# Kernel optimization log

Hardware: AMD Instinct MI355X
Metric: run time of the kernel (lower is better)

The kernel has to match this reference:

```python
import jax, jax.numpy as jnp
import numpy as np

N_USERS = 100000
N_ITEMS = 50000
N_NODES = N_USERS + N_ITEMS
N_EDGES = 4800000
EMB_DIM = 64
N_LAYERS = 3


def setup_inputs() -> dict:
    key = jax.random.key(0)
    k1, k2, k3, k4, k5 = jax.random.split(key, 5)
    adj_rows = jax.random.randint(k1, (N_EDGES,), 0, N_NODES, dtype=jnp.int64 if jax.config.jax_enable_x64 else jnp.int32)
    adj_cols = jax.random.randint(k2, (N_EDGES,), 0, N_NODES, dtype=jnp.int64 if jax.config.jax_enable_x64 else jnp.int32)
    adj_vals = jax.random.uniform(k3, (N_EDGES,), dtype=jnp.float32)
    user_emb = jax.random.normal(k4, (N_USERS, EMB_DIM), dtype=jnp.float32)
    item_emb = jax.random.normal(k5, (N_ITEMS, EMB_DIM), dtype=jnp.float32)
    return {"adj_rows": adj_rows, "adj_cols": adj_cols, "adj_vals": adj_vals,
            "user_emb": user_emb, "item_emb": item_emb}


def _spmm(rows, cols, vals, x):
    # sparse.mm(adj, x): gather source node features, scale by edge value,
    # scatter-add into destination rows. Shapes: [E] indices, [N, D] features.
    msgs = vals[:, None] * x[cols]          # [E, D]
    return jax.ops.segment_sum(msgs, rows, num_segments=N_NODES)  # [N, D]


def reference(adj_rows, adj_cols, adj_vals, user_emb, item_emb):
    all_emb = jnp.concatenate([user_emb, item_emb], axis=0)  # [N, D]
    acc = all_emb                                            # running sum over layers (fused stack+mean)
    emb = all_emb
    for _ in range(N_LAYERS):
        emb = _spmm(adj_rows, adj_cols, adj_vals, emb)
        acc = acc + emb
    final = acc / jnp.asarray(N_LAYERS + 1, dtype=acc.dtype)
    return final[:N_USERS], final[N_USERS:]
```

## Files before the change

kernel.cpp:

```cpp
#include <hip/hip_runtime.h>


#define N_USERS 100000
#define N_ITEMS 50000
#define N_NODES 150000
#define N_EDGES 4800000
#define EMB_DIM 64

typedef unsigned short u16;
typedef unsigned int   u32;

constexpr int NODE_FLOATS  = N_NODES * EMB_DIM;
constexpr int NODE_FLOAT4S = NODE_FLOATS / 4;
constexpr int USER_FLOAT4S = N_USERS * EMB_DIM / 4;

constexpr int BSH  = 7;
constexpr int BRW  = 128;
constexpr int NB   = (N_NODES + BRW - 1) / BRW;
constexpr int EPB  = 6144;
constexpr int ABLK2 = (N_EDGES + EPB - 1) / EPB;
constexpr int HSW  = NB + 1;
constexpr int SB_CAP2 = 5760;
constexpr int CSR_CAP = 6000000;

static __device__ __forceinline__ float bf2f(u16 b) {
    return __uint_as_float(((u32)b) << 16);
}
static __device__ __forceinline__ u16 f2bf(float f) {
    u32 u = __float_as_uint(f);
    return (u16)((u + 0x7FFFu + ((u >> 16) & 1u)) >> 16);
}

__global__ void prelude_kernel(const float* __restrict__ user_emb,
                               const float* __restrict__ item_emb,
                               u16* __restrict__ emb,
                               int* __restrict__ csr_cursor) {
    int i = blockIdx.x * blockDim.x + threadIdx.x;
    if (i == 0) csr_cursor[0] = 0;
    if (i >= NODE_FLOAT4S) return;
    float4 v = (i < USER_FLOAT4S) ? ((const float4*)user_emb)[i]
                                  : ((const float4*)item_emb)[i - USER_FLOAT4S];
    ushort4 o;
    o.x = f2bf(v.x); o.y = f2bf(v.y); o.z = f2bf(v.z); o.w = f2bf(v.w);
    ((ushort4*)emb)[i] = o;
}

__global__ void stageA2_kernel(const int* __restrict__ rows,
                               const int* __restrict__ cols,
                               const float* __restrict__ vals,
                               uint2* __restrict__ stage_rec,
                               u32* __restrict__ hs) {
    __shared__ u32 lkey[EPB];
    __shared__ u16 lval[EPB];
    __shared__ u16 lbkt[EPB];
    __shared__ int hist[NB];
    __shared__ int hstart[NB];
    __shared__ int hcur[NB];
    __shared__ int ws4[4];

    const int tid  = threadIdx.x;
    const int base = blockIdx.x * EPB;
    const int cnt  = min(EPB, N_EDGES - base);

    for (int i = tid; i < NB; i += 256) hist[i] = 0;
    __syncthreads();

    for (int k = 0; k < EPB / 256; k += 8) {
        int rbuf[8];
        #pragma unroll
        for (int q = 0; q < 8; ++q) {
            int idx = (k + q) * 256 + tid;
            rbuf[q] = (idx < cnt) ? rows[base + idx] : -1;
        }
        #pragma unroll
        for (int q = 0; q < 8; ++q)
            if (rbuf[q] >= 0) atomicAdd(&hist[rbuf[q] >> BSH], 1);
    }
    __syncthreads();

    const int lane = tid & 63, wave = tid >> 6;
    int carry = 0;
    for (int c0 = 0; c0 < NB; c0 += 256) {
        int i = c0 + tid;
        int v = (i < NB) ? hist[i] : 0;
        int incl = v;
        #pragma unroll
        for (int off = 1; off < 64; off <<= 1) {
            int t = __shfl_up(incl, off);
            if (lane >= off) incl += t;
        }
        if (lane == 63) ws4[wave] = incl;
        __syncthreads();
        int wpref = 0, tot = 0;
        #pragma unroll
        for (int w = 0; w < 4; ++w) { int s = ws4[w]; if (w < wave) wpref += s; tot += s; }
        int excl = carry + wpref + incl - v;
        if (i < NB) { hstart[i] = excl; hcur[i] = excl; }
        carry += tot;
        __syncthreads();
    }

    for (int k = 0; k < EPB / 256; k += 8) {
        int rb[8], cb[8]; float vb[8];
        #pragma unroll
        for (int q = 0; q < 8; ++q) {
            int idx = (k + q) * 256 + tid;
            if (idx < cnt) { rb[q] = rows[base + idx]; cb[q] = cols[base + idx]; vb[q] = vals[base + idx]; }
            else rb[q] = -1;
        }
        #pragma unroll
        for (int q = 0; q < 8; ++q) {
            if (rb[q] < 0) continue;
            int b = rb[q] >> BSH;
            int p = atomicAdd(&hcur[b], 1);
            lkey[p] = ((u32)(rb[q] & (BRW - 1)) << 24) | (u32)cb[q];
            lval[p] = f2bf(vb[q]);
            lbkt[p] = (u16)b;
        }
    }
    __syncthreads();
    (void)lbkt;

    uint2* __restrict__ dst = stage_rec + (size_t)blockIdx.x * EPB;
    for (int i = tid; i < cnt; i += 256)
        dst[i] = make_uint2(lkey[i], (u32)lval[i]);

    u32* __restrict__ hrow = hs + (size_t)blockIdx.x * HSW;
    for (int i = tid; i < NB; i += 256) hrow[i] = (u32)hstart[i];
    if (tid == 0) hrow[NB] = (u32)cnt;
}

__global__ void stageB2_kernel(const uint2* __restrict__ stage_rec,
                               const u32* __restrict__ hs,
                               int* __restrict__ csr_cursor,
                               u32* __restrict__ csr_col,
                               u16* __restrict__ csr_val,
                               u32* __restrict__ desc) {
    __shared__ u32 skey[SB_CAP2];
    __shared__ u16 sval[SB_CAP2];
    __shared__ int rhist[256], rpad0[256], rcur[256];
    __shared__ int ws4[4];
    __shared__ int sbase_sh;

    const int b   = blockIdx.x;
    const int tid = threadIdx.x;
    rhist[tid] = 0;
    __syncthreads();

    for (int a = tid; a < ABLK2; a += 256) {
        const u32* hp = hs + (size_t)a * HSW + b;
        u32 s = hp[0], e = hp[1];
        const uint2* rp = stage_rec + (size_t)a * EPB;
        for (u32 i = s; i < e; ++i)
            atomicAdd(&rhist[rp[i].x >> 24], 1);
    }
    __syncthreads();

    const int lane = tid & 63, wave = tid >> 6;
    int v  = rhist[tid];
    int vp = (v + 15) & ~15;
    int incl = vp;
    #pragma unroll
    for (int off = 1; off < 64; off <<= 1) {
        int t = __shfl_up(incl, off);
        if (lane >= off) incl += t;
    }
    if (lane == 63) ws4[wave] = incl;
    __syncthreads();
    int wpref = 0, total = 0;
    #pragma unroll
    for (int w = 0; w < 4; ++w) { int s = ws4[w]; if (w < wave) wpref += s; total += s; }
    int excl = wpref + incl - vp;
    rpad0[tid] = excl;
    rcur[tid]  = excl;
    if (tid == 0) sbase_sh = atomicAdd(csr_cursor, total);
    __syncthreads();

    const int tcap = min(total, SB_CAP2);
    for (int i = tid; i < tcap; i += 256) { skey[i] = 0u; sval[i] = 0; }
    __syncthreads();

    for (int a = tid; a < ABLK2; a += 256) {
        const u32* hp = hs + (size_t)a * HSW + b;
        u32 s = hp[0], e = hp[1];
        const uint2* rp = stage_rec + (size_t)a * EPB;
        for (u32 i = s; i < e; ++i) {
            uint2 r = rp[i];
            int p = atomicAdd(&rcur[r.x >> 24], 1);
            if (p < SB_CAP2) { skey[p] = r.x & 0x00FFFFFFu; sval[p] = (u16)r.y; }
        }
    }
    __syncthreads();

    const int sbase = sbase_sh;
    for (int i = tid; i < tcap; i += 256) {
        int g = sbase + i;
        if (g < CSR_CAP) { csr_col[g] = skey[i]; csr_val[g] = sval[i]; }
    }
    if (tid < BRW) {
        int grow = b * BRW + tid;
        if (grow < N_NODES) {
            int cp = vp; if (cp > 240) cp = 240;
            desc[grow] = ((u32)(sbase + rpad0[tid]) << 8) | (u32)cp;
        }
    }
}

__global__ __launch_bounds__(256, 8)
void spmm_rw_kernel(const u32* __restrict__ desc,
                    const u32* __restrict__ csr_col,
                    const u16* __restrict__ csr_val,
                    const u16* __restrict__ x,
                    u16* __restrict__ y,
                    const u16* __restrict__ e0,
                    const u16* __restrict__ y1,
                    const u16* __restrict__ y2,
                    float* __restrict__ out) {
    const int lane = threadIdx.x & 63;
    const int wid  = __builtin_amdgcn_readfirstlane(threadIdx.x >> 6);
    const int row  = blockIdx.x * 4 + wid;
    if (row >= N_NODES) return;

    const u32 d   = desc[row];
    const int beg = (int)(d >> 8);
    const int nch = (int)(d & 255u) >> 4;

    const u32* __restrict__ pc = csr_col + beg;
    const u32* __restrict__ pv = ((const u32*)csr_val) + (beg >> 1);
    const u16* __restrict__ xl = x + lane;

    float a[4] = {0.f, 0.f, 0.f, 0.f};

    for (int ch = 0; ch < nch; ++ch) {
        u32 c[16];
        u32 w[8];
        #pragma unroll
        for (int k = 0; k < 16; ++k) c[k] = pc[ch * 16 + k];
        #pragma unroll
        for (int k = 0; k < 8; ++k)  w[k] = pv[ch * 8 + k];

        u32 xv[16];
        #pragma unroll
        for (int k = 0; k < 16; ++k)
            xv[k] = (u32)xl[(size_t)c[k] * EMB_DIM];

        #pragma unroll
        for (int k = 0; k < 16; ++k) {
            u32 vb = (k & 1) ? (w[k >> 1] & 0xFFFF0000u) : (w[k >> 1] << 16);
            float vv = __uint_as_float(vb);
            float xf = __uint_as_float(xv[k] << 16);
            a[k & 3] += vv * xf;
        }
    }
    float s = (a[0] + a[1]) + (a[2] + a[3]);

    size_t oidx = (size_t)row * EMB_DIM + lane;
    if (y) {
        y[oidx] = f2bf(s);
    } else {
        float r = (bf2f(e0[oidx]) + bf2f(y1[oidx]) + bf2f(y2[oidx]) + s) * 0.25f;
        out[oidx] = r;
    }
}

__global__ void init3_kernel(const float* __restrict__ user_emb,
                             const float* __restrict__ item_emb,
                             float* __restrict__ emb,
                             float* __restrict__ acc,
                             float* __restrict__ nxt) {
    int i = blockIdx.x * blockDim.x + threadIdx.x;
    if (i >= NODE_FLOAT4S) return;
    float4 v = (i < USER_FLOAT4S) ? ((const float4*)user_emb)[i]
                                  : ((const float4*)item_emb)[i - USER_FLOAT4S];
    ((float4*)emb)[i] = v;
    ((float4*)acc)[i] = v;
    ((float4*)nxt)[i] = make_float4(0.f, 0.f, 0.f, 0.f);
}

__global__ void spmm_atomic_kernel(const int* __restrict__ rows,
                                   const int* __restrict__ cols,
                                   const float* __restrict__ vals,
                                   const float* __restrict__ x,
                                   float* __restrict__ y) {
    unsigned tid = blockIdx.x * blockDim.x + threadIdx.x;
    unsigned e  = tid >> 4;
    unsigned d4 = tid & 15u;
    if (e >= N_EDGES) return;
    int r = rows[e]; int c = cols[e]; float v = vals[e];
    float4 xv = ((const float4*)(x + (size_t)c * EMB_DIM))[d4];
    float* yp = y + (size_t)r * EMB_DIM + d4 * 4;
    atomicAdd(yp + 0, v * xv.x);
    atomicAdd(yp + 1, v * xv.y);
    atomicAdd(yp + 2, v * xv.z);
    atomicAdd(yp + 3, v * xv.w);
}

__global__ void acc_kernel(float* __restrict__ acc, const float* __restrict__ nxt,
                           float* __restrict__ zbuf, int do_zero, float scale) {
    int i = blockIdx.x * blockDim.x + threadIdx.x;
    if (i >= NODE_FLOAT4S) return;
    float4 a = ((float4*)acc)[i];
    float4 n = ((const float4*)nxt)[i];
    a.x = (a.x + n.x) * scale; a.y = (a.y + n.y) * scale;
    a.z = (a.z + n.z) * scale; a.w = (a.w + n.w) * scale;
    ((float4*)acc)[i] = a;
    if (do_zero) ((float4*)zbuf)[i] = make_float4(0.f, 0.f, 0.f, 0.f);
}

extern "C" void kernel_launch(void* const* d_in, const int* in_sizes, int n_in,
                              void* d_out, int out_size, void* d_ws, size_t ws_size,
                              hipStream_t stream) {
    const int*   rows     = (const int*)d_in[0];
    const int*   cols     = (const int*)d_in[1];
    const float* vals     = (const float*)d_in[2];
    const float* user_emb = (const float*)d_in[3];
    const float* item_emb = (const float*)d_in[4];
    float* out = (float*)d_out;

    constexpr size_t U_BUF  = (size_t)NODE_FLOATS / 2;
    constexpr size_t U_SREC = (size_t)ABLK2 * EPB * 2;
    constexpr size_t U_HS   = (size_t)ABLK2 * HSW;
    constexpr size_t U_CCOL = (size_t)CSR_CAP;
    constexpr size_t U_CVAL = (size_t)CSR_CAP / 2;
    size_t need_u32 = U_BUF + U_SREC + U_HS + U_CCOL + U_CVAL + (size_t)N_NODES + 16;

    const int EW_BLOCKS = (NODE_FLOAT4S + 255) / 256;

    if (ws_size >= need_u32 * 4) {
        u32* W = (u32*)d_ws;
        u16*   buf0      = (u16*)W;
        uint2* stage_rec = (uint2*)(W + U_BUF);
        u16*   buf1      = (u16*)(W + U_BUF);
        u16*   buf2      = (u16*)(W + U_BUF + U_BUF);
        u32*   hs        = W + U_BUF + U_SREC;
        u32*   csr_col   = hs + U_HS;
        u16*   csr_val   = (u16*)(csr_col + U_CCOL);
        u32*   desc      = (u32*)(csr_col + U_CCOL + U_CVAL);
        int*   csr_cur   = (int*)(desc + N_NODES);

        prelude_kernel<<<EW_BLOCKS, 256, 0, stream>>>(user_emb, item_emb, buf0, csr_cur);
        stageA2_kernel<<<ABLK2, 256, 0, stream>>>(rows, cols, vals, stage_rec, hs);
        stageB2_kernel<<<NB, 256, 0, stream>>>(stage_rec, hs, csr_cur,
                                               csr_col, csr_val, desc);

        const int SPMM_BLOCKS = (N_NODES + 3) / 4;
        spmm_rw_kernel<<<SPMM_BLOCKS, 256, 0, stream>>>(desc, csr_col, csr_val,
                                                        buf0, buf1, nullptr, nullptr, nullptr, nullptr);
        spmm_rw_kernel<<<SPMM_BLOCKS, 256, 0, stream>>>(desc, csr_col, csr_val,
                                                        buf1, buf2, nullptr, nullptr, nullptr, nullptr);
        spmm_rw_kernel<<<SPMM_BLOCKS, 256, 0, stream>>>(desc, csr_col, csr_val,
                                                        buf2, nullptr, buf0, buf1, buf2, out);
    } else {
        float* buf0 = (float*)d_ws;
        float* buf1 = buf0 + NODE_FLOATS;
        const int SPMM_BLOCKS = (int)(((size_t)N_EDGES * 16 + 255) / 256);
        init3_kernel<<<EW_BLOCKS, 256, 0, stream>>>(user_emb, item_emb, buf0, out, buf1);
        float* prev = buf0; float* next = buf1;
        for (int layer = 0; layer < 3; ++layer) {
            spmm_atomic_kernel<<<SPMM_BLOCKS, 256, 0, stream>>>(rows, cols, vals, prev, next);
            if (layer < 2) acc_kernel<<<EW_BLOCKS, 256, 0, stream>>>(out, next, prev, 1, 1.0f);
            else           acc_kernel<<<EW_BLOCKS, 256, 0, stream>>>(out, next, prev, 0, 0.25f);
            float* t = prev; prev = next; next = t;
        }
    }
}
```

Baseline: 522.1 us.

## Build CSR with degree count, scan and atomic scatter instead of bucket sort

Replaces the two-pass, shared-memory bucket sort that staged edge records with a simpler CSR build. Per-row degrees are counted with global atomics inside the prelude, then padded and prefix-scanned in two small kernels. Each edge is then placed by an atomic cursor per row. This drops the large staging buffer and the heavy LDS-bound sort kernels. In exchange it adds many random global atomics and scattered writes, plus a zeroing pass over the CSR arrays for the padding slots.

```diff
diff --git a/kernel.cpp b/kernel.cpp
--- a/kernel.cpp
+++ b/kernel.cpp
@@ -14,14 +14,9 @@
 constexpr int NODE_FLOAT4S = NODE_FLOATS / 4;
 constexpr int USER_FLOAT4S = N_USERS * EMB_DIM / 4;
 
-constexpr int BSH  = 7;
-constexpr int BRW  = 128;
-constexpr int NB   = (N_NODES + BRW - 1) / BRW;
-constexpr int EPB  = 6144;
-constexpr int ABLK2 = (N_EDGES + EPB - 1) / EPB;
-constexpr int HSW  = NB + 1;
-constexpr int SB_CAP2 = 5760;
-constexpr int CSR_CAP = 6000000;
+constexpr int SCAN_BLK  = 147;
+constexpr int ROWS_PAD  = SCAN_BLK * 1024;
+constexpr int CSR_CAP   = 6200000;
 
 static __device__ __forceinline__ float bf2f(u16 b) {
     return __uint_as_float(((u32)b) << 16);
@@ -31,178 +26,94 @@
     return (u16)((u + 0x7FFFu + ((u >> 16) & 1u)) >> 16);
 }
 
+constexpr size_t U_CCOL = (size_t)CSR_CAP;
+constexpr size_t U_CVAL = (size_t)CSR_CAP / 2;
+constexpr size_t U_DEG  = (size_t)ROWS_PAD;
+constexpr size_t U_CUR  = (size_t)ROWS_PAD;
+constexpr size_t ZU32   = U_CCOL + U_CVAL + U_DEG + U_CUR;
+
+__global__ void zero_kernel(uint4* __restrict__ z) {
+    size_t i = (size_t)blockIdx.x * blockDim.x + threadIdx.x;
+    if (i < ZU32 / 4) z[i] = make_uint4(0u, 0u, 0u, 0u);
+}
+
 __global__ void prelude_kernel(const float* __restrict__ user_emb,
                                const float* __restrict__ item_emb,
                                u16* __restrict__ emb,
-                               int* __restrict__ csr_cursor) {
+                               const int* __restrict__ rows,
+                               u32* __restrict__ deg) {
     int i = blockIdx.x * blockDim.x + threadIdx.x;
-    if (i == 0) csr_cursor[0] = 0;
     if (i >= NODE_FLOAT4S) return;
     float4 v = (i < USER_FLOAT4S) ? ((const float4*)user_emb)[i]
                                   : ((const float4*)item_emb)[i - USER_FLOAT4S];
     ushort4 o;
     o.x = f2bf(v.x); o.y = f2bf(v.y); o.z = f2bf(v.z); o.w = f2bf(v.w);
     ((ushort4*)emb)[i] = o;
-}
-
-__global__ void stageA2_kernel(const int* __restrict__ rows,
-                               const int* __restrict__ cols,
-                               const float* __restrict__ vals,
-                               uint2* __restrict__ stage_rec,
-                               u32* __restrict__ hs) {
-    __shared__ u32 lkey[EPB];
-    __shared__ u16 lval[EPB];
-    __shared__ u16 lbkt[EPB];
-    __shared__ int hist[NB];
-    __shared__ int hstart[NB];
-    __shared__ int hcur[NB];
-    __shared__ int ws4[4];
-
-    const int tid  = threadIdx.x;
-    const int base = blockIdx.x * EPB;
-    const int cnt  = min(EPB, N_EDGES - base);
-
-    for (int i = tid; i < NB; i += 256) hist[i] = 0;
-    __syncthreads();
-
-    for (int k = 0; k < EPB / 256; k += 8) {
-        int rbuf[8];
-        #pragma unroll
-        for (int q = 0; q < 8; ++q) {
-            int idx = (k + q) * 256 + tid;
-            rbuf[q] = (idx < cnt) ? rows[base + idx] : -1;
-        }
-        #pragma unroll
-        for (int q = 0; q < 8; ++q)
-            if (rbuf[q] >= 0) atomicAdd(&hist[rbuf[q] >> BSH], 1);
-    }
-    __syncthreads();
-
-    const int lane = tid & 63, wave = tid >> 6;
-    int carry = 0;
-    for (int c0 = 0; c0 < NB; c0 += 256) {
-        int i = c0 + tid;
-        int v = (i < NB) ? hist[i] : 0;
-        int incl = v;
-        #pragma unroll
-        for (int off = 1; off < 64; off <<= 1) {
-            int t = __shfl_up(incl, off);
-            if (lane >= off) incl += t;
-        }
-        if (lane == 63) ws4[wave] = incl;
-        __syncthreads();
-        int wpref = 0, tot = 0;
-        #pragma unroll
-        for (int w = 0; w < 4; ++w) { int s = ws4[w]; if (w < wave) wpref += s; tot += s; }
-        int excl = carry + wpref + incl - v;
-        if (i < NB) { hstart[i] = excl; hcur[i] = excl; }
-        carry += tot;
-        __syncthreads();
-    }
-
-    for (int k = 0; k < EPB / 256; k += 8) {
-        int rb[8], cb[8]; float vb[8];
-        #pragma unroll
-        for (int q = 0; q < 8; ++q) {
-            int idx = (k + q) * 256 + tid;
-            if (idx < cnt) { rb[q] = rows[base + idx]; cb[q] = cols[base + idx]; vb[q] = vals[base + idx]; }
-            else rb[q] = -1;
-        }
-        #pragma unroll
-        for (int q = 0; q < 8; ++q) {
-            if (rb[q] < 0) continue;
-            int b = rb[q] >> BSH;
-            int p = atomicAdd(&hcur[b], 1);
-            lkey[p] = ((u32)(rb[q] & (BRW - 1)) << 24) | (u32)cb[q];
-            lval[p] = f2bf(vb[q]);
-            lbkt[p] = (u16)b;
-        }
-    }
-    __syncthreads();
-    (void)lbkt;
-
-    uint2* __restrict__ dst = stage_rec + (size_t)blockIdx.x * EPB;
-    for (int i = tid; i < cnt; i += 256)
-        dst[i] = make_uint2(lkey[i], (u32)lval[i]);
-
-    u32* __restrict__ hrow = hs + (size_t)blockIdx.x * HSW;
-    for (int i = tid; i < NB; i += 256) hrow[i] = (u32)hstart[i];
-    if (tid == 0) hrow[NB] = (u32)cnt;
-}
-
-__global__ void stageB2_kernel(const uint2* __restrict__ stage_rec,
-                               const u32* __restrict__ hs,
-                               int* __restrict__ csr_cursor,
-                               u32* __restrict__ csr_col,
-                               u16* __restrict__ csr_val,
-                               u32* __restrict__ desc) {
-    __shared__ u32 skey[SB_CAP2];
-    __shared__ u16 sval[SB_CAP2];
-    __shared__ int rhist[256], rpad0[256], rcur[256];
-    __shared__ int ws4[4];
-    __shared__ int sbase_sh;
-
-    const int b   = blockIdx.x;
+    atomicAdd(&deg[rows[i]], 1u);
+    atomicAdd(&deg[rows[i + NODE_FLOAT4S]], 1u);
+}
+
+__global__ __launch_bounds__(1024)
+void scanA_kernel(u32* __restrict__ deg_desc, u32* __restrict__ blocksum) {
+    __shared__ int wsum[16], wbase[16];
     const int tid = threadIdx.x;
-    rhist[tid] = 0;
-    __syncthreads();
-
-    for (int a = tid; a < ABLK2; a += 256) {
-        const u32* hp = hs + (size_t)a * HSW + b;
-        u32 s = hp[0], e = hp[1];
-        const uint2* rp = stage_rec + (size_t)a * EPB;
-        for (u32 i = s; i < e; ++i)
-            atomicAdd(&rhist[rp[i].x >> 24], 1);
-    }
-    __syncthreads();
-
-    const int lane = tid & 63, wave = tid >> 6;
-    int v  = rhist[tid];
-    int vp = (v + 15) & ~15;
+    const int row = blockIdx.x * 1024 + tid;
+    const int lane = tid & 63, wv = tid >> 6;
+
+    int d  = (int)deg_desc[row];
+    int vp = (d + 15) & ~15;
+
     int incl = vp;
     #pragma unroll
     for (int off = 1; off < 64; off <<= 1) {
         int t = __shfl_up(incl, off);
         if (lane >= off) incl += t;
     }
-    if (lane == 63) ws4[wave] = incl;
+    if (lane == 63) wsum[wv] = incl;
     __syncthreads();
-    int wpref = 0, total = 0;
-    #pragma unroll
-    for (int w = 0; w < 4; ++w) { int s = ws4[w]; if (w < wave) wpref += s; total += s; }
-    int excl = wpref + incl - vp;
-    rpad0[tid] = excl;
-    rcur[tid]  = excl;
-    if (tid == 0) sbase_sh = atomicAdd(csr_cursor, total);
+    if (tid < 16) {
+        int s = wsum[tid];
+        int i2 = s;
+        #pragma unroll
+        for (int off = 1; off < 16; off <<= 1) {
+            int t = __shfl_up(i2, off);
+            if (lane >= off) i2 += t;
+        }
+        wbase[tid] = i2 - s;
+        if (tid == 15) blocksum[blockIdx.x] = (u32)i2;
+    }
     __syncthreads();
 
-    const int tcap = min(total, SB_CAP2);
-    for (int i = tid; i < tcap; i += 256) { skey[i] = 0u; sval[i] = 0; }
-    __syncthreads();
-
-    for (int a = tid; a < ABLK2; a += 256) {
-        const u32* hp = hs + (size_t)a * HSW + b;
-        u32 s = hp[0], e = hp[1];
-        const uint2* rp = stage_rec + (size_t)a * EPB;
-        for (u32 i = s; i < e; ++i) {
-            uint2 r = rp[i];
-            int p = atomicAdd(&rcur[r.x >> 24], 1);
-            if (p < SB_CAP2) { skey[p] = r.x & 0x00FFFFFFu; sval[p] = (u16)r.y; }
-        }
-    }
-    __syncthreads();
-
-    const int sbase = sbase_sh;
-    for (int i = tid; i < tcap; i += 256) {
-        int g = sbase + i;
-        if (g < CSR_CAP) { csr_col[g] = skey[i]; csr_val[g] = sval[i]; }
-    }
-    if (tid < BRW) {
-        int grow = b * BRW + tid;
-        if (grow < N_NODES) {
-            int cp = vp; if (cp > 240) cp = 240;
-            desc[grow] = ((u32)(sbase + rpad0[tid]) << 8) | (u32)cp;
-        }
+    int excl = wbase[wv] + incl - vp;
+    int cnt  = vp > 240 ? 240 : vp;
+    deg_desc[row] = ((u32)excl << 8) | (u32)cnt;
+}
+
+__global__ __launch_bounds__(1024)
+void scanC_kernel(u32* __restrict__ desc, const u32* __restrict__ blocksum) {
+    const int blk = blockIdx.x;
+    u32 base = 0;
+    for (int i = 0; i < blk; ++i) base += blocksum[i];
+    const int row = blk * 1024 + threadIdx.x;
+    desc[row] += base << 8;
+}
+
+__global__ void scatter_kernel(const int* __restrict__ rows,
+                               const int* __restrict__ cols,
+                               const float* __restrict__ vals,
+                               const u32* __restrict__ desc,
+                               u32* __restrict__ cursor,
+                               u32* __restrict__ csr_col,
+                               u16* __restrict__ csr_val) {
+    int e = blockIdx.x * blockDim.x + threadIdx.x;
+    if (e >= N_EDGES) return;
+    int r = rows[e];
+    u32 dsc = desc[r];
+    u32 pos = atomicAdd(&cursor[r], 1u);
+    u32 g = (dsc >> 8) + pos;
+    if (g < (u32)CSR_CAP) {
+        csr_col[g] = (u32)cols[e];
+        csr_val[g] = f2bf(vals[e]);
     }
 }
 
@@ -317,38 +228,38 @@
     const float* item_emb = (const float*)d_in[4];
     float* out = (float*)d_out;
 
-    constexpr size_t U_BUF  = (size_t)NODE_FLOATS / 2;
-    constexpr size_t U_SREC = (size_t)ABLK2 * EPB * 2;
-    constexpr size_t U_HS   = (size_t)ABLK2 * HSW;
-    constexpr size_t U_CCOL = (size_t)CSR_CAP;
-    constexpr size_t U_CVAL = (size_t)CSR_CAP / 2;
-    size_t need_u32 = U_BUF + U_SREC + U_HS + U_CCOL + U_CVAL + (size_t)N_NODES + 16;
+    constexpr size_t U_BUF = (size_t)NODE_FLOATS / 2;
+    size_t need_u32 = 3 * U_BUF + ZU32 + 160;
 
     const int EW_BLOCKS = (NODE_FLOAT4S + 255) / 256;
 
     if (ws_size >= need_u32 * 4) {
         u32* W = (u32*)d_ws;
-        u16*   buf0      = (u16*)W;
-        uint2* stage_rec = (uint2*)(W + U_BUF);
-        u16*   buf1      = (u16*)(W + U_BUF);
-        u16*   buf2      = (u16*)(W + U_BUF + U_BUF);
-        u32*   hs        = W + U_BUF + U_SREC;
-        u32*   csr_col   = hs + U_HS;
-        u16*   csr_val   = (u16*)(csr_col + U_CCOL);
-        u32*   desc      = (u32*)(csr_col + U_CCOL + U_CVAL);
-        int*   csr_cur   = (int*)(desc + N_NODES);
-
-        prelude_kernel<<<EW_BLOCKS, 256, 0, stream>>>(user_emb, item_emb, buf0, csr_cur);
-        stageA2_kernel<<<ABLK2, 256, 0, stream>>>(rows, cols, vals, stage_rec, hs);
-        stageB2_kernel<<<NB, 256, 0, stream>>>(stage_rec, hs, csr_cur,
-                                               csr_col, csr_val, desc);
+        u16* buf0     = (u16*)W;
+        u16* buf1     = (u16*)(W + U_BUF);
+        u16* buf2     = (u16*)(W + 2 * U_BUF);
+        u32* csr_col  = W + 3 * U_BUF;
+        u16* csr_val  = (u16*)(csr_col + U_CCOL);
+        u32* deg_desc = csr_col + U_CCOL + U_CVAL;
+        u32* cursor   = deg_desc + U_DEG;
+        u32* blocksum = cursor + U_CUR;
+
+        const int ZBLOCKS = (int)((ZU32 / 4 + 255) / 256);
+        zero_kernel<<<ZBLOCKS, 256, 0, stream>>>((uint4*)csr_col);
+        prelude_kernel<<<EW_BLOCKS, 256, 0, stream>>>(user_emb, item_emb, buf0,
+                                                      rows, deg_desc);
+        scanA_kernel<<<SCAN_BLK, 1024, 0, stream>>>(deg_desc, blocksum);
+        scanC_kernel<<<SCAN_BLK, 1024, 0, stream>>>(deg_desc, blocksum);
+        const int SCAT_BLOCKS = (N_EDGES + 255) / 256;
+        scatter_kernel<<<SCAT_BLOCKS, 256, 0, stream>>>(rows, cols, vals, deg_desc,
+                                                        cursor, csr_col, csr_val);
 
         const int SPMM_BLOCKS = (N_NODES + 3) / 4;
-        spmm_rw_kernel<<<SPMM_BLOCKS, 256, 0, stream>>>(desc, csr_col, csr_val,
+        spmm_rw_kernel<<<SPMM_BLOCKS, 256, 0, stream>>>(deg_desc, csr_col, csr_val,
                                                         buf0, buf1, nullptr, nullptr, nullptr, nullptr);
-        spmm_rw_kernel<<<SPMM_BLOCKS, 256, 0, stream>>>(desc, csr_col, csr_val,
+        spmm_rw_kernel<<<SPMM_BLOCKS, 256, 0, stream>>>(deg_desc, csr_col, csr_val,
                                                         buf1, buf2, nullptr, nullptr, nullptr, nullptr);
-        spmm_rw_kernel<<<SPMM_BLOCKS, 256, 0, stream>>>(desc, csr_col, csr_val,
+        spmm_rw_kernel<<<SPMM_BLOCKS, 256, 0, stream>>>(deg_desc, csr_col, csr_val,
                                                         buf2, nullptr, buf0, buf1, buf2, out);
     } else {
         float* buf0 = (float*)d_ws;
```

Measured after the change: 908.5 us. 1.74x slower.

## Replace two-pass bucket CSR build with global-atomic partition scatter into fixed slots

Applied to the files above, without the earlier changes.

The CSR build changes from per-block staging records plus a per-bucket scan over every staging block to a partitioned scheme. Each stage-A block reserves space in 512-row partitions with a global atomic and scatters its records directly into fixed-capacity partition buffers. A 512-thread stage-B block per partition then counting-sorts its own contiguous buffer into fixed-offset CSR slots. This removes stage B's loop over all ABLK2 blocks' headers and its scattered small reads, but it introduces fixed capacities (PCAP, PCSR) that drop edges silently if a partition overflows, and it pads every row inside fixed partition strides.

```diff
diff --git a/kernel.cpp b/kernel.cpp
--- a/kernel.cpp
+++ b/kernel.cpp
@@ -14,14 +14,13 @@
 constexpr int NODE_FLOAT4S = NODE_FLOATS / 4;
 constexpr int USER_FLOAT4S = N_USERS * EMB_DIM / 4;
 
-constexpr int BSH  = 7;
-constexpr int BRW  = 128;
-constexpr int NB   = (N_NODES + BRW - 1) / BRW;
-constexpr int EPB  = 6144;
+constexpr int PSH   = 9;
+constexpr int PRW   = 512;
+constexpr int NP    = (N_NODES + PRW - 1) / PRW;
+constexpr int PCAP  = 17920;
+constexpr int PCSR  = 22528;
+constexpr int EPB   = 6144;
 constexpr int ABLK2 = (N_EDGES + EPB - 1) / EPB;
-constexpr int HSW  = NB + 1;
-constexpr int SB_CAP2 = 5760;
-constexpr int CSR_CAP = 6000000;
 
 static __device__ __forceinline__ float bf2f(u16 b) {
     return __uint_as_float(((u32)b) << 16);
@@ -34,9 +33,9 @@
 __global__ void prelude_kernel(const float* __restrict__ user_emb,
                                const float* __restrict__ item_emb,
                                u16* __restrict__ emb,
-                               int* __restrict__ csr_cursor) {
+                               int* __restrict__ pcnt) {
     int i = blockIdx.x * blockDim.x + threadIdx.x;
-    if (i == 0) csr_cursor[0] = 0;
+    if (i < 512) pcnt[i] = 0;
     if (i >= NODE_FLOAT4S) return;
     float4 v = (i < USER_FLOAT4S) ? ((const float4*)user_emb)[i]
                                   : ((const float4*)item_emb)[i - USER_FLOAT4S];
@@ -45,24 +44,22 @@
     ((ushort4*)emb)[i] = o;
 }
 
-__global__ void stageA2_kernel(const int* __restrict__ rows,
-                               const int* __restrict__ cols,
-                               const float* __restrict__ vals,
-                               uint2* __restrict__ stage_rec,
-                               u32* __restrict__ hs) {
+__global__ void stageP_kernel(const int* __restrict__ rows,
+                              const int* __restrict__ cols,
+                              const float* __restrict__ vals,
+                              int* __restrict__ pcnt,
+                              uint2* __restrict__ part_buf) {
     __shared__ u32 lkey[EPB];
     __shared__ u16 lval[EPB];
     __shared__ u16 lbkt[EPB];
-    __shared__ int hist[NB];
-    __shared__ int hstart[NB];
-    __shared__ int hcur[NB];
+    __shared__ int hist[NP], hstart[NP], hcur[NP], gbase[NP];
     __shared__ int ws4[4];
 
     const int tid  = threadIdx.x;
     const int base = blockIdx.x * EPB;
     const int cnt  = min(EPB, N_EDGES - base);
 
-    for (int i = tid; i < NB; i += 256) hist[i] = 0;
+    for (int i = tid; i < NP; i += 256) hist[i] = 0;
     __syncthreads();
 
     for (int k = 0; k < EPB / 256; k += 8) {
@@ -74,15 +71,15 @@
         }
         #pragma unroll
         for (int q = 0; q < 8; ++q)
-            if (rbuf[q] >= 0) atomicAdd(&hist[rbuf[q] >> BSH], 1);
+            if (rbuf[q] >= 0) atomicAdd(&hist[rbuf[q] >> PSH], 1);
     }
     __syncthreads();
 
     const int lane = tid & 63, wave = tid >> 6;
     int carry = 0;
-    for (int c0 = 0; c0 < NB; c0 += 256) {
+    for (int c0 = 0; c0 < NP; c0 += 256) {
         int i = c0 + tid;
-        int v = (i < NB) ? hist[i] : 0;
+        int v = (i < NP) ? hist[i] : 0;
         int incl = v;
         #pragma unroll
         for (int off = 1; off < 64; off <<= 1) {
@@ -95,7 +92,7 @@
         #pragma unroll
         for (int w = 0; w < 4; ++w) { int s = ws4[w]; if (w < wave) wpref += s; tot += s; }
         int excl = carry + wpref + incl - v;
-        if (i < NB) { hstart[i] = excl; hcur[i] = excl; }
+        if (i < NP) { hstart[i] = excl; hcur[i] = excl; }
         carry += tot;
         __syncthreads();
     }
@@ -111,52 +108,55 @@
         #pragma unroll
         for (int q = 0; q < 8; ++q) {
             if (rb[q] < 0) continue;
-            int b = rb[q] >> BSH;
+            int b = rb[q] >> PSH;
             int p = atomicAdd(&hcur[b], 1);
-            lkey[p] = ((u32)(rb[q] & (BRW - 1)) << 24) | (u32)cb[q];
+            lkey[p] = ((u32)(rb[q] & (PRW - 1)) << 18) | (u32)cb[q];
             lval[p] = f2bf(vb[q]);
             lbkt[p] = (u16)b;
         }
     }
     __syncthreads();
-    (void)lbkt;
-
-    uint2* __restrict__ dst = stage_rec + (size_t)blockIdx.x * EPB;
-    for (int i = tid; i < cnt; i += 256)
-        dst[i] = make_uint2(lkey[i], (u32)lval[i]);
-
-    u32* __restrict__ hrow = hs + (size_t)blockIdx.x * HSW;
-    for (int i = tid; i < NB; i += 256) hrow[i] = (u32)hstart[i];
-    if (tid == 0) hrow[NB] = (u32)cnt;
-}
-
-__global__ void stageB2_kernel(const uint2* __restrict__ stage_rec,
-                               const u32* __restrict__ hs,
-                               int* __restrict__ csr_cursor,
-                               u32* __restrict__ csr_col,
-                               u16* __restrict__ csr_val,
-                               u32* __restrict__ desc) {
-    __shared__ u32 skey[SB_CAP2];
-    __shared__ u16 sval[SB_CAP2];
-    __shared__ int rhist[256], rpad0[256], rcur[256];
-    __shared__ int ws4[4];
-    __shared__ int sbase_sh;
-
-    const int b   = blockIdx.x;
+
+    for (int i = tid; i < NP; i += 256) {
+        int n = hist[i];
+        if (n) {
+            int p = atomicAdd(&pcnt[i], n);
+            gbase[i] = (p + n <= PCAP) ? p : -1;
+        }
+    }
+    __syncthreads();
+
+    for (int i = tid; i < cnt; i += 256) {
+        int b  = lbkt[i];
+        int gb = gbase[b];
+        if (gb >= 0)
+            part_buf[(size_t)b * PCAP + gb + (i - hstart[b])] =
+                make_uint2(lkey[i], (u32)lval[i]);
+    }
+}
+
+__global__ __launch_bounds__(512)
+void stageB_kernel(const int* __restrict__ pcnt,
+                   const uint2* __restrict__ part_buf,
+                   u32* __restrict__ csr_col,
+                   u16* __restrict__ csr_val,
+                   u32* __restrict__ desc) {
+    __shared__ int rhist[PRW], rcur[PRW];
+    __shared__ int wsum[8];
+
+    const int p   = blockIdx.x;
     const int tid = threadIdx.x;
     rhist[tid] = 0;
     __syncthreads();
 
-    for (int a = tid; a < ABLK2; a += 256) {
-        const u32* hp = hs + (size_t)a * HSW + b;
-        u32 s = hp[0], e = hp[1];
-        const uint2* rp = stage_rec + (size_t)a * EPB;
-        for (u32 i = s; i < e; ++i)
-            atomicAdd(&rhist[rp[i].x >> 24], 1);
-    }
-    __syncthreads();
-
-    const int lane = tid & 63, wave = tid >> 6;
+    const int n = min(pcnt[p], PCAP);
+    const uint2* __restrict__ rp = part_buf + (size_t)p * PCAP;
+
+    for (int i = tid; i < n; i += 512)
+        atomicAdd(&rhist[rp[i].x >> 18], 1);
+    __syncthreads();
+
+    const int lane = tid & 63, wv = tid >> 6;
     int v  = rhist[tid];
     int vp = (v + 15) & ~15;
     int incl = vp;
@@ -165,43 +165,35 @@
         int t = __shfl_up(incl, off);
         if (lane >= off) incl += t;
     }
-    if (lane == 63) ws4[wave] = incl;
-    __syncthreads();
-    int wpref = 0, total = 0;
+    if (lane == 63) wsum[wv] = incl;
+    __syncthreads();
+    int wpref = 0;
     #pragma unroll
-    for (int w = 0; w < 4; ++w) { int s = ws4[w]; if (w < wave) wpref += s; total += s; }
+    for (int w = 0; w < 8; ++w) { int s = wsum[w]; if (w < wv) wpref += s; }
     int excl = wpref + incl - vp;
-    rpad0[tid] = excl;
-    rcur[tid]  = excl;
-    if (tid == 0) sbase_sh = atomicAdd(csr_cursor, total);
-    __syncthreads();
-
-    const int tcap = min(total, SB_CAP2);
-    for (int i = tid; i < tcap; i += 256) { skey[i] = 0u; sval[i] = 0; }
-    __syncthreads();
-
-    for (int a = tid; a < ABLK2; a += 256) {
-        const u32* hp = hs + (size_t)a * HSW + b;
-        u32 s = hp[0], e = hp[1];
-        const uint2* rp = stage_rec + (size_t)a * EPB;
-        for (u32 i = s; i < e; ++i) {
-            uint2 r = rp[i];
-            int p = atomicAdd(&rcur[r.x >> 24], 1);
-            if (p < SB_CAP2) { skey[p] = r.x & 0x00FFFFFFu; sval[p] = (u16)r.y; }
-        }
-    }
-    __syncthreads();
-
-    const int sbase = sbase_sh;
-    for (int i = tid; i < tcap; i += 256) {
-        int g = sbase + i;
-        if (g < CSR_CAP) { csr_col[g] = skey[i]; csr_val[g] = sval[i]; }
-    }
-    if (tid < BRW) {
-        int grow = b * BRW + tid;
-        if (grow < N_NODES) {
-            int cp = vp; if (cp > 240) cp = 240;
-            desc[grow] = ((u32)(sbase + rpad0[tid]) << 8) | (u32)cp;
+    rcur[tid] = excl;
+
+    const int cbase = p * PCSR;
+    int grow = p * PRW + tid;
+    if (grow < N_NODES && excl + vp <= PCSR) {
+        int cp = vp > 240 ? 240 : vp;
+        desc[grow] = ((u32)(cbase + excl) << 8) | (u32)cp;
+    } else if (grow < N_NODES) {
+        desc[grow] = ((u32)cbase << 8);
+    }
+    for (int j = v; j < vp; ++j) {
+        int g = excl + j;
+        if (g < PCSR) { csr_col[cbase + g] = 0u; csr_val[cbase + g] = 0; }
+    }
+    __syncthreads();
+
+    for (int i = tid; i < n; i += 512) {
+        uint2 r = rp[i];
+        int rl  = (int)(r.x >> 18);
+        int pos = atomicAdd(&rcur[rl], 1);
+        if (pos < PCSR) {
+            csr_col[cbase + pos] = r.x & 0x3FFFFu;
+            csr_val[cbase + pos] = (u16)r.y;
         }
     }
 }
@@ -318,30 +310,29 @@
     float* out = (float*)d_out;
 
     constexpr size_t U_BUF  = (size_t)NODE_FLOATS / 2;
-    constexpr size_t U_SREC = (size_t)ABLK2 * EPB * 2;
-    constexpr size_t U_HS   = (size_t)ABLK2 * HSW;
-    constexpr size_t U_CCOL = (size_t)CSR_CAP;
-    constexpr size_t U_CVAL = (size_t)CSR_CAP / 2;
-    size_t need_u32 = U_BUF + U_SREC + U_HS + U_CCOL + U_CVAL + (size_t)N_NODES + 16;
+    constexpr size_t U_PART = (size_t)NP * PCAP * 2;
+    constexpr size_t U_X    = U_PART;
+    constexpr size_t U_CCOL = (size_t)NP * PCSR;
+    constexpr size_t U_CVAL = U_CCOL / 2;
+    constexpr size_t U_DESC = 150528;
+    size_t need_u32 = U_BUF + U_X + U_CCOL + U_CVAL + U_DESC + 512;
 
     const int EW_BLOCKS = (NODE_FLOAT4S + 255) / 256;
 
     if (ws_size >= need_u32 * 4) {
-        u32* W = (u32*)d_ws;
-        u16*   buf0      = (u16*)W;
-        uint2* stage_rec = (uint2*)(W + U_BUF);
-        u16*   buf1      = (u16*)(W + U_BUF);
-        u16*   buf2      = (u16*)(W + U_BUF + U_BUF);
-        u32*   hs        = W + U_BUF + U_SREC;
-        u32*   csr_col   = hs + U_HS;
-        u16*   csr_val   = (u16*)(csr_col + U_CCOL);
-        u32*   desc      = (u32*)(csr_col + U_CCOL + U_CVAL);
-        int*   csr_cur   = (int*)(desc + N_NODES);
-
-        prelude_kernel<<<EW_BLOCKS, 256, 0, stream>>>(user_emb, item_emb, buf0, csr_cur);
-        stageA2_kernel<<<ABLK2, 256, 0, stream>>>(rows, cols, vals, stage_rec, hs);
-        stageB2_kernel<<<NB, 256, 0, stream>>>(stage_rec, hs, csr_cur,
-                                               csr_col, csr_val, desc);
+        u32*   W        = (u32*)d_ws;
+        u16*   buf0     = (u16*)W;
+        uint2* part_buf = (uint2*)(W + U_BUF);
+        u16*   buf1     = (u16*)(W + U_BUF);
+        u16*   buf2     = (u16*)(W + U_BUF + U_BUF);
+        u32*   csr_col  = W + U_BUF + U_X;
+        u16*   csr_val  = (u16*)(csr_col + U_CCOL);
+        u32*   desc     = (u32*)(csr_col + U_CCOL + U_CVAL);
+        int*   pcnt     = (int*)(desc + U_DESC);
+
+        prelude_kernel<<<EW_BLOCKS, 256, 0, stream>>>(user_emb, item_emb, buf0, pcnt);
+        stageP_kernel<<<ABLK2, 256, 0, stream>>>(rows, cols, vals, pcnt, part_buf);
+        stageB_kernel<<<NP, 512, 0, stream>>>(pcnt, part_buf, csr_col, csr_val, desc);
 
         const int SPMM_BLOCKS = (N_NODES + 3) / 4;
         spmm_rw_kernel<<<SPMM_BLOCKS, 256, 0, stream>>>(desc, csr_col, csr_val,
```

Measured after the change: 526.6 us. About the same (+0.9%).
